# Kernel optimization log

Hardware: AMD Instinct MI355X
Metric: run time of the kernel (lower is better)

Reference implementation:

```python
import jax, jax.numpy as jnp
import numpy as np

N_NODES = 50000
N_EDGES = 800000
EPS = 1e-5


def _layer_norm(h, gamma, beta):
    mu = jnp.mean(h, axis=-1, keepdims=True)
    var = jnp.var(h, axis=-1, keepdims=True)
    return (h - mu) * jax.lax.rsqrt(var + EPS) * gamma + beta


def _sage_layer(h, src, tgt, Wl, bl, Wr, gamma, beta):
    # mean-aggregate neighbor features at target nodes
    agg = jax.ops.segment_sum(h[src], tgt, num_segments=N_NODES)
    cnt = jax.ops.segment_sum(jnp.ones((src.shape[0],), h.dtype), tgt, num_segments=N_NODES)
    agg = agg / jnp.clip(cnt, 1.0, None)[:, None]
    # SAGEConv: lin_l(agg) + lin_r(x); lin_r has no bias
    out = agg @ Wl + bl + h @ Wr
    return jax.nn.relu(_layer_norm(out, gamma, beta))


def _xavier(key, shape):
    fan_in, fan_out = shape
    lim = float(np.sqrt(6.0 / (fan_in + fan_out)))
    return jax.random.uniform(key, shape, jnp.float32, -lim, lim)


def setup_inputs() -> dict:
    key = jax.random.key(0)
    ks = jax.random.split(key, 10)
    x = jax.random.normal(ks[0], (N_NODES, 84), jnp.float32)
    edge_index = jax.random.randint(ks[1], (2, N_EDGES), 0, N_NODES, jnp.int64)
    return {
        "x": x,
        "edge_index": edge_index,
        "W_in": _xavier(ks[2], (84, 128)), "b_in": jnp.zeros((128,), jnp.float32),
        "Wl1": _xavier(ks[3], (128, 64)), "bl1": jnp.zeros((64,), jnp.float32),
        "Wr1": _xavier(ks[4], (128, 64)),
        "g1": jnp.ones((64,), jnp.float32), "be1": jnp.zeros((64,), jnp.float32),
        "Wl2": _xavier(ks[5], (64, 32)), "bl2": jnp.zeros((32,), jnp.float32),
        "Wr2": _xavier(ks[6], (64, 32)),
        "g2": jnp.ones((32,), jnp.float32), "be2": jnp.zeros((32,), jnp.float32),
        "Wo1": _xavier(ks[7], (32, 16)), "bo1": jnp.zeros((16,), jnp.float32),
        "Wo2": _xavier(ks[8], (16, 1)), "bo2": jnp.zeros((1,), jnp.float32),
    }


def reference(x, edge_index, W_in, b_in, Wl1, bl1, Wr1, g1, be1,
              Wl2, bl2, Wr2, g2, be2, Wo1, bo1, Wo2, bo2):
    src, tgt = edge_index[0], edge_index[1]
    # input projection (dropout = identity in eval)
    h = jax.nn.relu(x @ W_in + b_in)                    # [N, 128]
    # GraphSAGE stack
    h = _sage_layer(h, src, tgt, Wl1, bl1, Wr1, g1, be1)  # [N, 64]
    h = _sage_layer(h, src, tgt, Wl2, bl2, Wr2, g2, be2)  # [N, 32]
    # output projection MLP
    h2 = jax.nn.relu(h @ Wo1 + bo1)                     # [N, 16]
    node_predictions = h2 @ Wo2 + bo2                   # [N, 1]
    return node_predictions
```

## Files before the change

### kernel.cpp

```cpp
#include <hip/hip_runtime.h>
#include <hip/hip_bf16.h>
#include <hip/hip_fp16.h>

#define NN 50000
#define NE 800000
#define EPS 1e-5f
#define NW 782
#define CAP 2560
#define WFB 200
#define CHUNK (NE / WFB)
#define PREPB 64
#define INPB ((NN + 31) / 32)

typedef _Float16 f16;
typedef _Float16 f16x8 __attribute__((ext_vector_type(8)));
typedef float f32x4 __attribute__((ext_vector_type(4)));

__device__ __forceinline__ int waveInclScan(int v, int lane) {
#pragma unroll
    for (int o = 1; o < 64; o <<= 1) {
        int t = __shfl_up(v, o, 64);
        if (lane >= o) v += t;
    }
    return v;
}

__global__ __launch_bounds__(256) void k_prep_init(const float* __restrict__ Win,
                                                   const float* __restrict__ Wl,
                                                   const float* __restrict__ Wr,
                                                   const float* __restrict__ Wl2,
                                                   const float* __restrict__ Wr2,
                                                   const float* __restrict__ Wo1,
                                                   f16* __restrict__ WinT,
                                                   f16* __restrict__ W2T,
                                                   f16* __restrict__ W3T,
                                                   f16* __restrict__ Wo1T,
                                                   int* __restrict__ wcur) {
    int i0 = blockIdx.x * 256 + threadIdx.x;
    for (int i = i0; i < 128 * 104; i += PREPB * 256) {
        int c = i / 104, k = i - c * 104;
        float v = (k < 84) ? Win[k * 128 + c] : 0.f;
        WinT[c * 104 + k] = (f16)v;
    }
    for (int i = i0; i < 128 * 136; i += PREPB * 256) {
        int c = i / 136, k = i - c * 136;
        float v = 0.f;
        if (k < 128) v = (c < 64) ? Wl[k * 64 + c] : Wr[k * 64 + (c - 64)];
        W2T[c * 136 + k] = (f16)v;
    }
    for (int i = i0; i < 64 * 72; i += PREPB * 256) {
        int c = i / 72, k = i - c * 72;
        float v = 0.f;
        if (k < 64) v = (c < 32) ? Wl2[k * 32 + c] : Wr2[k * 32 + (c - 32)];
        W3T[c * 72 + k] = (f16)v;
    }
    for (int i = i0; i < 16 * 40; i += PREPB * 256) {
        int c = i / 40, k = i - c * 40;
        float v = (k < 32) ? Wo1[k * 16 + c] : 0.f;
        Wo1T[c * 40 + k] = (f16)v;
    }
    for (int i = i0; i < NW; i += PREPB * 256) wcur[i] = i * CAP;
}

__global__ __launch_bounds__(256) void k_wfill_inproj(const int* __restrict__ src,
                                                      const int* __restrict__ tgt,
                                                      int* __restrict__ wcur,
                                                      int* __restrict__ colw,
                                                      const float* __restrict__ x,
                                                      const f16* __restrict__ WinT,
                                                      const float* __restrict__ bin,
                                                      const f16* __restrict__ W2T,
                                                      const float* __restrict__ bl,
                                                      f16* __restrict__ p1h,
                                                      f16* __restrict__ r1h, int N) {
    __shared__ int lh[NW];
    __shared__ int sb[NW];
    __shared__ __align__(16) f16 xs[32 * 104];
    __shared__ __align__(16) f16 hs[32 * 136];
    int tid = threadIdx.x;

    if (blockIdx.x < WFB) {
        int i4lo = (blockIdx.x * CHUNK) >> 2;
        int i4hi = i4lo + (CHUNK >> 2);
        for (int i = tid; i < NW; i += 256) lh[i] = 0;
        __syncthreads();
        for (int i4 = i4lo + tid; i4 < i4hi; i4 += 256) {
            int4 t = ((const int4*)tgt)[i4];
            atomicAdd(&lh[t.x >> 6], 1);
            atomicAdd(&lh[t.y >> 6], 1);
            atomicAdd(&lh[t.z >> 6], 1);
            atomicAdd(&lh[t.w >> 6], 1);
        }
        __syncthreads();
        for (int i = tid; i < NW; i += 256) {
            int c = lh[i];
            sb[i] = c ? atomicAdd(&wcur[i], c) : 0;
            lh[i] = 0;
        }
        __syncthreads();
        for (int i4 = i4lo + tid; i4 < i4hi; i4 += 256) {
            int4 t = ((const int4*)tgt)[i4];
            int4 s = ((const int4*)src)[i4];
            int w0 = t.x >> 6, r0 = atomicAdd(&lh[w0], 1);
            colw[sb[w0] + r0] = (s.x << 6) | (t.x & 63);
            int w1 = t.y >> 6, r1 = atomicAdd(&lh[w1], 1);
            colw[sb[w1] + r1] = (s.y << 6) | (t.y & 63);
            int w2 = t.z >> 6, r2 = atomicAdd(&lh[w2], 1);
            colw[sb[w2] + r2] = (s.z << 6) | (t.z & 63);
            int w3 = t.w >> 6, r3 = atomicAdd(&lh[w3], 1);
            colw[sb[w3] + r3] = (s.w << 6) | (t.w & 63);
        }
        return;
    }

    int node0 = (blockIdx.x - WFB) * 32;
    int lane = tid & 63;
    int wv = tid >> 6;
    int r = lane & 15;
    int q = lane >> 4;

    f16x8 b1[2][3];
#pragma unroll
    for (int nt = 0; nt < 2; nt++) {
        int c = (2 * wv + nt) * 16 + r;
#pragma unroll
        for (int ks = 0; ks < 3; ks++)
            b1[nt][ks] = *(const f16x8*)&WinT[c * 104 + ks * 32 + q * 8];
    }
    for (int i = tid; i < 672; i += 256) {
        int nd = i / 21, k4 = i - nd * 21;
        int g = node0 + nd;
        float4 v = make_float4(0.f, 0.f, 0.f, 0.f);
        if (g < N) v = ((const float4*)x)[(size_t)g * 21 + k4];
        f16* dst = &xs[nd * 104 + k4 * 4];
        dst[0] = (f16)v.x; dst[1] = (f16)v.y; dst[2] = (f16)v.z; dst[3] = (f16)v.w;
    }
    for (int i = tid; i < 32 * 12; i += 256) {
        int nd = i / 12, k = 84 + (i - nd * 12);
        xs[nd * 104 + k] = (f16)0.f;
    }
    __syncthreads();

    f32x4 acc[2][2] = {};
#pragma unroll
    for (int ks = 0; ks < 3; ks++) {
        int k0 = ks * 32;
        f16x8 a[2];
#pragma unroll
        for (int mt = 0; mt < 2; mt++)
            a[mt] = *(const f16x8*)&xs[(mt * 16 + r) * 104 + k0 + q * 8];
#pragma unroll
        for (int mt = 0; mt < 2; mt++)
#pragma unroll
            for (int nt = 0; nt < 2; nt++)
                acc[mt][nt] = __builtin_amdgcn_mfma_f32_16x16x32_f16(a[mt], b1[nt][ks], acc[mt][nt], 0, 0, 0);
    }

    f16x8 b2[2][4];
#pragma unroll
    for (int nt = 0; nt < 2; nt++) {
        int c = (2 * wv + nt) * 16 + r;
#pragma unroll
        for (int ks = 0; ks < 4; ks++)
            b2[nt][ks] = *(const f16x8*)&W2T[c * 136 + ks * 32 + q * 8];
    }

#pragma unroll
    for (int nt = 0; nt < 2; nt++) {
        int c = (2 * wv + nt) * 16 + r;
        float bb = bin[c];
#pragma unroll
        for (int mt = 0; mt < 2; mt++)
#pragma unroll
            for (int v = 0; v < 4; v++) {
                int row = mt * 16 + q * 4 + v;
                float val = acc[mt][nt][v] + bb;
                hs[row * 136 + c] = (f16)(val > 0.f ? val : 0.f);
            }
    }
    __syncthreads();

    f32x4 acc2[2][2] = {};
#pragma unroll
    for (int ks = 0; ks < 4; ks++) {
        int k0 = ks * 32;
        f16x8 a[2];
#pragma unroll
        for (int mt = 0; mt < 2; mt++)
            a[mt] = *(const f16x8*)&hs[(mt * 16 + r) * 136 + k0 + q * 8];
#pragma unroll
        for (int mt = 0; mt < 2; mt++)
#pragma unroll
            for (int nt = 0; nt < 2; nt++)
                acc2[mt][nt] = __builtin_amdgcn_mfma_f32_16x16x32_f16(a[mt], b2[nt][ks], acc2[mt][nt], 0, 0, 0);
    }

#pragma unroll
    for (int nt = 0; nt < 2; nt++) {
        int c = (2 * wv + nt) * 16 + r;
        float bb = (c >= 64) ? bl[c - 64] : 0.f;
#pragma unroll
        for (int mt = 0; mt < 2; mt++)
#pragma unroll
            for (int v = 0; v < 4; v++) {
                int n = node0 + mt * 16 + q * 4 + v;
                if (n < N) {
                    float val = acc2[mt][nt][v];
                    if (c < 64) p1h[(size_t)n * 64 + c] = (f16)val;
                    else        r1h[(size_t)n * 64 + (c - 64)] = (f16)(val + bb);
                }
            }
    }
}

#define F2ADD(a, b) { (a).x += (b).x; (a).y += (b).y; }

__global__ __launch_bounds__(512) void k_agg1_proj2(const __half2* __restrict__ p1v,
                                                    const __half2* __restrict__ r1v,
                                                    const int* __restrict__ wcur,
                                                    const int* __restrict__ colw,
                                                    const float* __restrict__ g1,
                                                    const float* __restrict__ be1,
                                                    const f16* __restrict__ W3T,
                                                    const float* __restrict__ bl2,
                                                    f16* __restrict__ p2h,
                                                    f16* __restrict__ r2h, int N) {
    __shared__ int cnt[64], start[64], cur[64];
    __shared__ int sorted[CAP];
    __shared__ __align__(16) f16 ys[64][72];
    int tid = threadIdx.x;
    int wb = blockIdx.x;
    int base = wb * CAP;
    int nb = wb << 6;
    int len = wcur[wb] - base;
    if (len > CAP) len = CAP;

    unsigned cc = tid & 31;
    int grp = tid >> 5;
    int lane = tid & 63;
    int wv = tid >> 6;
    int r = lane & 15;
    int q = lane >> 4;

    int mt = wv & 3;
    int ntbase = (wv >> 2) * 2;
    f16x8 b3[2][2];
#pragma unroll
    for (int j = 0; j < 2; j++)
#pragma unroll
        for (int ks = 0; ks < 2; ks++)
            b3[j][ks] = *(const f16x8*)&W3T[((ntbase + j) * 16 + r) * 72 + ks * 32 + q * 8];

    if (tid < 64) cnt[tid] = 0;
    __syncthreads();
    for (int i = tid; i < len; i += 512) atomicAdd(&cnt[colw[base + i] & 63], 1);
    __syncthreads();
    if (tid < 64) {
        int v = cnt[tid];
        int incl = waveInclScan(v, tid);
        start[tid] = incl - v;
        cur[tid] = incl - v;
    }
    __syncthreads();
    for (int i = tid; i < len; i += 512) {
        int pk = colw[base + i];
        int pos = atomicAdd(&cur[pk & 63], 1);
        sorted[pos] = pk >> 6;
    }
    __syncthreads();

#pragma unroll
    for (int t = 0; t < 4; t++) {
        int tl = grp + 16 * t;
        int n = nb + tl;
        if (n < N) {
            int s0 = start[tl], s1 = start[tl] + cnt[tl];
            float2 a0 = make_float2(0.f, 0.f), a1 = a0, a2 = a0, a3 = a0;
            float2 a4 = a0, a5 = a0, a6 = a0, a7 = a0;
            int i = s0;
            for (; i + 7 < s1; i += 8) {
                unsigned c0 = sorted[i],     c1 = sorted[i + 1], c2 = sorted[i + 2], c3 = sorted[i + 3];
                unsigned c4 = sorted[i + 4], c5 = sorted[i + 5], c6 = sorted[i + 6], c7 = sorted[i + 7];
                float2 v0 = __half22float2(p1v[c0 * 32u + cc]);
                float2 v1 = __half22float2(p1v[c1 * 32u + cc]);
                float2 v2 = __half22float2(p1v[c2 * 32u + cc]);
                float2 v3 = __half22float2(p1v[c3 * 32u + cc]);
                float2 v4 = __half22float2(p1v[c4 * 32u + cc]);
                float2 v5 = __half22float2(p1v[c5 * 32u + cc]);
                float2 v6 = __half22float2(p1v[c6 * 32u + cc]);
                float2 v7 = __half22float2(p1v[c7 * 32u + cc]);
                F2ADD(a0, v0) F2ADD(a1, v1) F2ADD(a2, v2) F2ADD(a3, v3)
                F2ADD(a4, v4) F2ADD(a5, v5) F2ADD(a6, v6) F2ADD(a7, v7)
            }
            for (; i < s1; i++) {
                float2 v0 = __half22float2(p1v[(unsigned)sorted[i] * 32u + cc]);
                F2ADD(a0, v0)
            }
            F2ADD(a0, a4) F2ADD(a1, a5) F2ADD(a2, a6) F2ADD(a3, a7)
            F2ADD(a0, a2) F2ADD(a1, a3) F2ADD(a0, a1)
            int cntv = s1 - s0;
            float inv = 1.f / (float)(cntv > 1 ? cntv : 1);
            float2 rr = __half22float2(r1v[(unsigned)n * 32u + cc]);
            float vx = a0.x * inv + rr.x;
            float vy = a0.y * inv + rr.y;
            float s = vx + vy;
#pragma unroll
            for (int o = 1; o < 32; o <<= 1) s += __shfl_xor(s, o, 32);
            float m = s * (1.f / 64.f);
            float dx = vx - m, dy = vy - m;
            float qv = dx * dx + dy * dy;
#pragma unroll
            for (int o = 1; o < 32; o <<= 1) qv += __shfl_xor(qv, o, 32);
            float rs = rsqrtf(qv * (1.f / 64.f) + EPS);
            float y0 = dx * rs * g1[2 * cc] + be1[2 * cc];
            float y1 = dy * rs * g1[2 * cc + 1] + be1[2 * cc + 1];
            ys[tl][2 * cc]     = (f16)(y0 > 0.f ? y0 : 0.f);
            ys[tl][2 * cc + 1] = (f16)(y1 > 0.f ? y1 : 0.f);
        } else {
            ys[tl][2 * cc] = (f16)0.f;
            ys[tl][2 * cc + 1] = (f16)0.f;
        }
    }
    __syncthreads();

#pragma unroll
    for (int j = 0; j < 2; j++) {
        int nt = ntbase + j;
        f32x4 acc = {};
#pragma unroll
        for (int ks = 0; ks < 2; ks++) {
            f16x8 a = *(const f16x8*)&ys[mt * 16 + r][ks * 32 + q * 8];
            acc = __builtin_amdgcn_mfma_f32_16x16x32_f16(a, b3[j][ks], acc, 0, 0, 0);
        }
        int c2 = nt * 16 + r;
        float bb = (c2 >= 32) ? bl2[c2 - 32] : 0.f;
#pragma unroll
        for (int v = 0; v < 4; v++) {
            int n = nb + mt * 16 + q * 4 + v;
            if (n < N) {
                float val = acc[v];
                if (c2 < 32) p2h[(size_t)n * 32 + c2] = (f16)val;
                else         r2h[(size_t)n * 32 + (c2 - 32)] = (f16)(val + bb);
            }
        }
    }
}

__global__ __launch_bounds__(512) void k_agg2_out(const __half2* __restrict__ p2v,
                                                  const __half2* __restrict__ r2v,
                                                  const int* __restrict__ wcur,
                                                  const int* __restrict__ colw,
                                                  const float* __restrict__ g2,
                                                  const float* __restrict__ be2,
                                                  const f16* __restrict__ Wo1T,
                                                  const float* __restrict__ bo1,
                                                  const float* __restrict__ Wo2,
                                                  const float* __restrict__ bo2,
                                                  float* __restrict__ out, int N) {
    __shared__ int cnt[64], start[64], cur[64];
    __shared__ int sorted[CAP];
    __shared__ __align__(16) f16 ys[64][40];
    int tid = threadIdx.x;
    int wb = blockIdx.x;
    int base = wb * CAP;
    int nb = wb << 6;
    int len = wcur[wb] - base;
    if (len > CAP) len = CAP;

    unsigned l = tid & 15;
    int grp = tid >> 4;
    int lane = tid & 63;
    int wv = tid >> 6;
    int r = lane & 15;
    int q = lane >> 4;

    f16x8 bo = *(const f16x8*)&Wo1T[r * 40 + q * 8];
    float b1v = bo1[r];
    float w2v = Wo2[r];

    if (tid < 64) cnt[tid] = 0;
    __syncthreads();
    for (int i = tid; i < len; i += 512) atomicAdd(&cnt[colw[base + i] & 63], 1);
    __syncthreads();
    if (tid < 64) {
        int v = cnt[tid];
        int incl = waveInclScan(v, tid);
        start[tid] = incl - v;
        cur[tid] = incl - v;
    }
    __syncthreads();
    for (int i = tid; i < len; i += 512) {
        int pk = colw[base + i];
        int pos = atomicAdd(&cur[pk & 63], 1);
        sorted[pos] = pk >> 6;
    }
    __syncthreads();

#pragma unroll
    for (int t = 0; t < 2; t++) {
        int tl = grp + 32 * t;
        int n = nb + tl;
        if (n < N) {
            int s0 = start[tl], s1 = start[tl] + cnt[tl];
            float2 a0 = make_float2(0.f, 0.f), a1 = a0, a2 = a0, a3 = a0;
            float2 a4 = a0, a5 = a0, a6 = a0, a7 = a0;
            int i = s0;
            for (; i + 7 < s1; i += 8) {
                unsigned c0 = sorted[i],     c1 = sorted[i + 1], c2 = sorted[i + 2], c3 = sorted[i + 3];
                unsigned c4 = sorted[i + 4], c5 = sorted[i + 5], c6 = sorted[i + 6], c7 = sorted[i + 7];
                float2 v0 = __half22float2(p2v[c0 * 16u + l]);
                float2 v1 = __half22float2(p2v[c1 * 16u + l]);
                float2 v2 = __half22float2(p2v[c2 * 16u + l]);
                float2 v3 = __half22float2(p2v[c3 * 16u + l]);
                float2 v4 = __half22float2(p2v[c4 * 16u + l]);
                float2 v5 = __half22float2(p2v[c5 * 16u + l]);
                float2 v6 = __half22float2(p2v[c6 * 16u + l]);
                float2 v7 = __half22float2(p2v[c7 * 16u + l]);
                F2ADD(a0, v0) F2ADD(a1, v1) F2ADD(a2, v2) F2ADD(a3, v3)
                F2ADD(a4, v4) F2ADD(a5, v5) F2ADD(a6, v6) F2ADD(a7, v7)
            }
            for (; i < s1; i++) {
                float2 v0 = __half22float2(p2v[(unsigned)sorted[i] * 16u + l]);
                F2ADD(a0, v0)
            }
            F2ADD(a0, a4) F2ADD(a1, a5) F2ADD(a2, a6) F2ADD(a3, a7)
            F2ADD(a0, a2) F2ADD(a1, a3) F2ADD(a0, a1)
            int cntv = s1 - s0;
            float inv = 1.f / (float)(cntv > 1 ? cntv : 1);
            float2 rr = __half22float2(r2v[(unsigned)n * 16u + l]);
            float vx = a0.x * inv + rr.x;
            float vy = a0.y * inv + rr.y;
            float s = vx + vy;
#pragma unroll
            for (int o = 1; o < 16; o <<= 1) s += __shfl_xor(s, o, 16);
            float m = s * (1.f / 32.f);
            float dx = vx - m, dy = vy - m;
            float qv = dx * dx + dy * dy;
#pragma unroll
            for (int o = 1; o < 16; o <<= 1) qv += __shfl_xor(qv, o, 16);
            float rs = rsqrtf(qv * (1.f / 32.f) + EPS);
            float y0 = dx * rs * g2[2 * l] + be2[2 * l];
            float y1 = dy * rs * g2[2 * l + 1] + be2[2 * l + 1];
            ys[tl][2 * l]     = (f16)(y0 > 0.f ? y0 : 0.f);
            ys[tl][2 * l + 1] = (f16)(y1 > 0.f ? y1 : 0.f);
        } else {
            ys[tl][2 * l] = (f16)0.f;
            ys[tl][2 * l + 1] = (f16)0.f;
        }
    }
    __syncthreads();

    if (wv < 4) {
        f16x8 a = *(const f16x8*)&ys[wv * 16 + r][q * 8];
        f32x4 acc = {};
        acc = __builtin_amdgcn_mfma_f32_16x16x32_f16(a, bo, acc, 0, 0, 0);
#pragma unroll
        for (int v = 0; v < 4; v++) {
            float h = acc[v] + b1v;
            h = h > 0.f ? h : 0.f;
            float contrib = h * w2v;
#pragma unroll
            for (int o = 1; o < 16; o <<= 1) contrib += __shfl_xor(contrib, o, 16);
            int n = nb + wv * 16 + q * 4 + v;
            if (r == 0 && n < N) out[n] = contrib + bo2[0];
        }
    }
}

extern "C" void kernel_launch(void* const* d_in, const int* in_sizes, int n_in,
                              void* d_out, int out_size, void* d_ws, size_t ws_size,
                              hipStream_t stream) {
    const float* x    = (const float*)d_in[0];
    const int*   ei   = (const int*)d_in[1];
    const float* W_in = (const float*)d_in[2];
    const float* b_in = (const float*)d_in[3];
    const float* Wl1  = (const float*)d_in[4];
    const float* bl1  = (const float*)d_in[5];
    const float* Wr1  = (const float*)d_in[6];
    const float* g1   = (const float*)d_in[7];
    const float* be1  = (const float*)d_in[8];
    const float* Wl2  = (const float*)d_in[9];
    const float* bl2  = (const float*)d_in[10];
    const float* Wr2  = (const float*)d_in[11];
    const float* g2   = (const float*)d_in[12];
    const float* be2  = (const float*)d_in[13];
    const float* Wo1  = (const float*)d_in[14];
    const float* bo1  = (const float*)d_in[15];
    const float* Wo2  = (const float*)d_in[16];
    const float* bo2  = (const float*)d_in[17];
    float* out = (float*)d_out;

    const int N = NN, E = NE;
    const int* src = ei;
    const int* tgt = ei + E;

    char* w = (char*)d_ws;
    int* wcur = (int*)w;  w += (size_t)NW * 4;
    w = (char*)(((uintptr_t)w + 15) & ~(uintptr_t)15);
    int* colw = (int*)w;  w += (size_t)NW * CAP * 4;
    f16* p1h  = (f16*)w;  w += (size_t)N * 64 * 2;
    f16* r1h  = (f16*)w;  w += (size_t)N * 64 * 2;
    f16* p2h  = (f16*)w;  w += (size_t)N * 32 * 2;
    f16* r2h  = (f16*)w;  w += (size_t)N * 32 * 2;
    f16* WinT = (f16*)w;  w += (size_t)128 * 104 * 2;
    f16* W2T  = (f16*)w;  w += (size_t)128 * 136 * 2;
    f16* W3T  = (f16*)w;  w += (size_t)64 * 72 * 2;
    f16* Wo1T = (f16*)w;  w += (size_t)16 * 40 * 2;

    k_prep_init<<<PREPB, 256, 0, stream>>>(W_in, Wl1, Wr1, Wl2, Wr2, Wo1,
                                           WinT, W2T, W3T, Wo1T, wcur);
    k_wfill_inproj<<<WFB + INPB, 256, 0, stream>>>(src, tgt, wcur, colw,
                                                   x, WinT, b_in, W2T, bl1, p1h, r1h, N);
    k_agg1_proj2<<<NW, 512, 0, stream>>>((const __half2*)p1h, (const __half2*)r1h,
                                         wcur, colw, g1, be1, W3T, bl2, p2h, r2h, N);
    k_agg2_out<<<NW, 512, 0, stream>>>((const __half2*)p2h, (const __half2*)r2h,
                                       wcur, colw, g2, be2, Wo1T, bo1, Wo2, bo2, out, N);
}
```

Measured before the change: 85.15 us.

## Stage projection output through LDS for vectorized stores and warm L2 before gathers

The projection kernel now writes its MFMA results into shared memory, then has each thread emit 16-byte vector stores of full rows for p1h and r1h. Before, it made scattered 2-byte per-element stores. Both aggregation kernels also start with a cooperative streaming read of a slice of the gathered feature array (p1 or p2), so that random neighbor gathers hit L2 instead of HBM. This adds extra read traffic and two block barriers. It also assumes the buffer sizes and the 8-blocks-per-slice mapping match the hardware's L2/XCD arrangement.

```diff
diff --git a/kernel.cpp b/kernel.cpp
--- a/kernel.cpp
+++ b/kernel.cpp
@@ -11,6 +11,7 @@
 #define CHUNK (NE / WFB)
 #define PREPB 64
 #define INPB ((NN + 31) / 32)
+#define NSLICE ((NW + 7) / 8)
 
 typedef _Float16 f16;
 typedef _Float16 f16x8 __attribute__((ext_vector_type(8)));
@@ -23,6 +24,20 @@
         if (lane >= o) v += t;
     }
     return v;
+}
+
+__device__ __forceinline__ void l2_warm(const uint4* __restrict__ buf, int total16,
+                                        int wb, int tid, int nthreads) {
+    int per = (total16 + NSLICE - 1) / NSLICE;
+    int lo = (wb >> 3) * per;
+    int hi = lo + per;
+    if (hi > total16) hi = total16;
+    unsigned acc = 0;
+    for (int i = lo + tid; i < hi; i += nthreads) {
+        uint4 v = buf[i];
+        acc ^= v.x ^ v.y ^ v.z ^ v.w;
+    }
+    asm volatile("" :: "v"(acc));
 }
 
 __global__ __launch_bounds__(256) void k_prep_init(const float* __restrict__ Win,
@@ -195,6 +210,7 @@
                 acc2[mt][nt] = __builtin_amdgcn_mfma_f32_16x16x32_f16(a[mt], b2[nt][ks], acc2[mt][nt], 0, 0, 0);
     }
 
+    __syncthreads();
 #pragma unroll
     for (int nt = 0; nt < 2; nt++) {
         int c = (2 * wv + nt) * 16 + r;
@@ -203,13 +219,20 @@
         for (int mt = 0; mt < 2; mt++)
 #pragma unroll
             for (int v = 0; v < 4; v++) {
-                int n = node0 + mt * 16 + q * 4 + v;
-                if (n < N) {
-                    float val = acc2[mt][nt][v];
-                    if (c < 64) p1h[(size_t)n * 64 + c] = (f16)val;
-                    else        r1h[(size_t)n * 64 + (c - 64)] = (f16)(val + bb);
-                }
-            }
+                int row = mt * 16 + q * 4 + v;
+                hs[row * 136 + c] = (f16)(acc2[mt][nt][v] + bb);
+            }
+    }
+    __syncthreads();
+    {
+        int row = tid >> 3, c8 = tid & 7;
+        int n = node0 + row;
+        if (n < N) {
+            f16x8 vp = *(const f16x8*)&hs[row * 136 + c8 * 8];
+            *(f16x8*)&p1h[(size_t)n * 64 + c8 * 8] = vp;
+            f16x8 vr = *(const f16x8*)&hs[row * 136 + 64 + c8 * 8];
+            *(f16x8*)&r1h[(size_t)n * 64 + c8 * 8] = vr;
+        }
     }
 }
 
@@ -234,6 +257,8 @@
     int nb = wb << 6;
     int len = wcur[wb] - base;
     if (len > CAP) len = CAP;
+
+    l2_warm((const uint4*)p1v, 229376, wb, tid, 512);
 
     unsigned cc = tid & 31;
     int grp = tid >> 5;
@@ -366,6 +391,8 @@
     int nb = wb << 6;
     int len = wcur[wb] - base;
     if (len > CAP) len = CAP;
+
+    l2_warm((const uint4*)p2v, 200000, wb, tid, 512);
 
     unsigned l = tid & 15;
     int grp = tid >> 4;
```

Measured after the change: 88.40 us. +3.8%, slower.
